# Kernel tuning notes

Hardware: AMD Instinct MI355X
Metric: run time of the kernel (lower is better)

The kernel has to match this reference:

```python
import jax, jax.numpy as jnp
import numpy as np
from jax import lax

B, N, C = 16, 131072, 3
NPOINT = 1024
OUT = 384
HID = OUT // 2


def farthest_point_sample(points, npoint):
    """points: [B, N, 3] -> idx: [B, npoint] int32 (classic FPS, start at index 0)."""
    b, n, _ = points.shape

    def body(carry, _):
        min_dist, last_idx = carry
        last = jnp.take_along_axis(points, last_idx[:, None, None], axis=1)  # [B,1,3]
        d = jnp.sum((points - last) ** 2, axis=-1)                           # [B,N]
        min_dist = jnp.minimum(min_dist, d)
        nxt = jnp.argmax(min_dist, axis=-1).astype(jnp.int32)
        return (min_dist, nxt), nxt

    idx0 = jnp.zeros((b,), jnp.int32)
    dist0 = jnp.full((b, n), 1e10, dtype=points.dtype)
    _, idxs = lax.scan(body, (dist0, idx0), None, length=npoint - 1)  # [npoint-1, B]
    return jnp.concatenate([idx0[None, :], idxs], axis=0).T           # [B, npoint]


def shared_mlp(x, w1, b1, w2, b2):
    # Conv1d(kernel_size=1) == pointwise linear; x: [B, M, Cin]
    h = jax.nn.gelu(jnp.einsum('bmc,ch->bmh', x, w1) + b1, approximate=False)
    return jnp.einsum('bmh,ho->bmo', h, w2) + b2


def setup_inputs() -> dict:
    key = jax.random.key(0)
    ks = jax.random.split(key, 9)
    points = jax.random.normal(ks[0], (B, N, C), dtype=jnp.float32)
    s1 = 1.0 / np.sqrt(C)
    s2 = 1.0 / np.sqrt(HID)
    return {
        'points': points,
        'w1t': jax.random.uniform(ks[1], (C, HID), jnp.float32, -s1, s1),
        'b1t': jax.random.uniform(ks[2], (HID,), jnp.float32, -s1, s1),
        'w2t': jax.random.uniform(ks[3], (HID, OUT), jnp.float32, -s2, s2),
        'b2t': jax.random.uniform(ks[4], (OUT,), jnp.float32, -s2, s2),
        'w1p': jax.random.uniform(ks[5], (C, HID), jnp.float32, -s1, s1),
        'b1p': jax.random.uniform(ks[6], (HID,), jnp.float32, -s1, s1),
        'w2p': jax.random.uniform(ks[7], (HID, OUT), jnp.float32, -s2, s2),
        'b2p': jax.random.uniform(ks[8], (OUT,), jnp.float32, -s2, s2),
    }


def reference(points, w1t, b1t, w2t, b2t, w1p, b1p, w2p, b2p):
    center_idx = farthest_point_sample(points, NPOINT)                      # [B, npoint]
    center = jnp.take_along_axis(points, center_idx[:, :, None], axis=1)   # [B, npoint, 3]
    det_token = shared_mlp(center, w1t, b1t, w2t, b2t)                      # [B, npoint, OUT]
    det_pos = shared_mlp(center, w1p, b1p, w2p, b2p)                        # [B, npoint, OUT]
    return det_token, det_pos
```

## Files before the change

### kernel.cpp

```cpp
#include <hip/hip_runtime.h>

#define NB 16
#define NPTS 131072
#define NPOINT 1024
#define HID 192
#define OUTC 384
#define BLKS_PER_B 16
#define THREADS_FPS 1024
#define PTS_PER_T 8
#define TAG_INIT 1023u
#define TAGM 0x3FFu

static __device__ __forceinline__ unsigned long long ald_ag(const unsigned long long* p) {
  return __hip_atomic_load(p, __ATOMIC_RELAXED, __HIP_MEMORY_SCOPE_AGENT);
}
static __device__ __forceinline__ void ast_ag(unsigned long long* p, unsigned long long v) {
  __hip_atomic_store(p, v, __ATOMIC_RELAXED, __HIP_MEMORY_SCOPE_AGENT);
}
__device__ __forceinline__ unsigned long long shfl_u64(unsigned long long v, int src) {
  unsigned int lo = (unsigned int)v, hi = (unsigned int)(v >> 32);
  lo = __shfl(lo, src, 64);
  hi = __shfl(hi, src, 64);
  return ((unsigned long long)hi << 32) | lo;
}
__device__ __forceinline__ unsigned long long shflxor_max_u64(unsigned long long v, int off) {
  unsigned int lo = (unsigned int)v, hi = (unsigned int)(v >> 32);
  lo = __shfl_xor(lo, off, 64);
  hi = __shfl_xor(hi, off, 64);
  unsigned long long o = ((unsigned long long)hi << 32) | lo;
  return o > v ? o : v;
}

__global__ __launch_bounds__(1024) void fps_kernel(
    const float* __restrict__ points,
    unsigned long long* __restrict__ slots,
    int* __restrict__ fps_idx)
{
  const int blk = blockIdx.x;
  const int b = blk >> 4;
  const int r = blk & 15;
  const int t = threadIdx.x;
  const int lane = t & 63, wid = t >> 6;
  const float* __restrict__ P = points + (size_t)b * NPTS * 3;
  const int base = r << 13;

  float px[PTS_PER_T], py[PTS_PER_T], pz[PTS_PER_T], md[PTS_PER_T];
#pragma unroll
  for (int k = 0; k < PTS_PER_T; ++k) {
    int i = base + (k << 10) + t;
    const float* pp = P + (size_t)i * 3;
    px[k] = pp[0]; py[k] = pp[1]; pz[k] = pp[2];
    md[k] = 1e10f;
  }

  float lx = P[0], ly = P[1], lz = P[2];

  __shared__ unsigned long long s_red[16];
  __shared__ float s_x[16], s_y[16], s_z[16];
  __shared__ float s_w[3];

  unsigned long long* region_b = slots + (size_t)b * 2 * 64;

  for (int it = 0; it < NPOINT - 1; ++it) {
    const int par = it & 1;
    const unsigned int uit = (unsigned int)it;
    const unsigned long long tg = (unsigned long long)uit;

    float bm = -1.0f; int bk = 0;
#pragma unroll
    for (int k = 0; k < PTS_PER_T; ++k) {
      float dx = px[k] - lx, dy = py[k] - ly, dz = pz[k] - lz;
      float d = __fadd_rn(__fadd_rn(__fmul_rn(dx, dx), __fmul_rn(dy, dy)), __fmul_rn(dz, dz));
      float m = fminf(md[k], d);
      md[k] = m;
      if (m > bm) { bm = m; bk = k; }
    }
    int bi = base + (bk << 10) + t;
    unsigned long long key = ((unsigned long long)__float_as_uint(bm) << 32)
                           | ((unsigned long long)(unsigned)(NPTS - 1 - bi) << 15);
#pragma unroll
    for (int off = 32; off > 0; off >>= 1) {
      unsigned int lo = (unsigned int)key, hi = (unsigned int)(key >> 32);
      lo = __shfl_down(lo, off, 64);
      hi = __shfl_down(hi, off, 64);
      unsigned long long o = ((unsigned long long)hi << 32) | lo;
      key = o > key ? o : key;
    }
    key = shfl_u64(key, 0);
    {
      int iw = NPTS - 1 - (int)((key >> 15) & 0x1FFFFull);
      int tw = (iw - base) & 1023;
      int kw = (iw - base) >> 10;
      float xc = px[0], yc = py[0], zc = pz[0];
#pragma unroll
      for (int k = 1; k < PTS_PER_T; ++k) {
        bool s = (kw == k);
        xc = s ? px[k] : xc; yc = s ? py[k] : yc; zc = s ? pz[k] : zc;
      }
      float xw = __shfl(xc, tw & 63, 64);
      float yw = __shfl(yc, tw & 63, 64);
      float zw = __shfl(zc, tw & 63, 64);
      if (lane == 0) {
        s_red[wid] = key;
        s_x[wid] = xw; s_y[wid] = yw; s_z[wid] = zw;
      }
    }
    __syncthreads();

    if (wid == 0) {
      unsigned long long kk = 0ull;
      if (lane < 16) {
        kk = s_red[lane];
#pragma unroll
        for (int off = 8; off > 0; off >>= 1) kk = shflxor_max_u64(kk, off);
      }
      kk = shfl_u64(kk, 0);
      int ib = NPTS - 1 - (int)((kk >> 15) & 0x1FFFFull);
      int wb = ((ib - base) & 1023) >> 6;
      unsigned long long* reg = region_b + (size_t)par * 64;
      if (lane < 4) {
        float cw = (lane == 1) ? s_x[wb] : (lane == 2) ? s_y[wb] : s_z[wb];
        unsigned long long w = (lane == 0)
            ? (kk | tg)
            : (((unsigned long long)__float_as_uint(cw) << 32) | tg);
        ast_ag(&reg[4 * r + lane], w);
      }
      unsigned long long* pp = reg + lane;
      unsigned long long pv;
      for (;;) {
        unsigned long long a0 = ald_ag(pp);
        unsigned long long a1 = ald_ag(pp);
        if (__ballot(((unsigned int)a0 & TAGM) == uit) == ~0ull) { pv = a0; break; }
        if (__ballot(((unsigned int)a1 & TAGM) == uit) == ~0ull) { pv = a1; break; }
        __builtin_amdgcn_s_sleep(2);
      }
      unsigned long long k4 = shfl_u64(pv, lane & ~3);
      k4 = shflxor_max_u64(k4, 4);
      k4 = shflxor_max_u64(k4, 8);
      k4 = shflxor_max_u64(k4, 16);
      k4 = shflxor_max_u64(k4, 32);
      int gi = NPTS - 1 - (int)((k4 >> 15) & 0x1FFFFull);
      int gr = gi >> 13;
      float myf = __uint_as_float((unsigned int)(pv >> 32));
      float nx = __shfl(myf, 4 * gr + 1, 64);
      float ny = __shfl(myf, 4 * gr + 2, 64);
      float nz = __shfl(myf, 4 * gr + 3, 64);
      if (lane == 0) {
        s_w[0] = nx; s_w[1] = ny; s_w[2] = nz;
        if (r == 0) fps_idx[b * NPOINT + it + 1] = gi;
      }
    }
    __syncthreads();
    lx = s_w[0]; ly = s_w[1]; lz = s_w[2];
  }
}

__global__ void fps_init_kernel(unsigned long long* __restrict__ slots,
                                int* __restrict__ fps_idx)
{
  int i = blockIdx.x * blockDim.x + threadIdx.x;
  if (i < NB * 2 * 64) slots[i] = (unsigned long long)TAG_INIT;
  if (i < NB) fps_idx[i * NPOINT] = 0;
}

__global__ __launch_bounds__(384) void mlp_kernel(
    const float* __restrict__ points,
    const int* __restrict__ fps_idx,
    const float* __restrict__ w1t, const float* __restrict__ b1t,
    const float* __restrict__ w2t, const float* __restrict__ b2t,
    const float* __restrict__ w1p, const float* __restrict__ b1p,
    const float* __restrict__ w2p, const float* __restrict__ b2p,
    float* __restrict__ out)
{
  __shared__ float s_c[4][3];
  __shared__ float s_h[2][HID][4];
  const int t = threadIdx.x;
  const int m0 = blockIdx.x * 4;
  if (t < 4) {
    int m = m0 + t;
    int b = m >> 10;
    int idx = fps_idx[m];
    const float* p = points + ((size_t)b * NPTS + (size_t)idx) * 3;
    s_c[t][0] = p[0]; s_c[t][1] = p[1]; s_c[t][2] = p[2];
  }
  __syncthreads();
  {
    const int mlp = t / HID;
    const int k = t - mlp * HID;
    const float* w1 = mlp ? w1p : w1t;
    const float* b1 = mlp ? b1p : b1t;
    float wa = w1[k], wb = w1[HID + k], wc = w1[2 * HID + k], bb = b1[k];
#pragma unroll
    for (int r = 0; r < 4; ++r) {
      float z = s_c[r][0] * wa + s_c[r][1] * wb + s_c[r][2] * wc + bb;
      float g = 0.5f * z * (1.0f + erff(z * 0.70710678118654752440f));
      s_h[mlp][k][r] = g;
    }
  }
  __syncthreads();
  const int o = t;
  float acct[4] = {0.f, 0.f, 0.f, 0.f};
  float accp[4] = {0.f, 0.f, 0.f, 0.f};
  const float* w2t_o = w2t + o;
  const float* w2p_o = w2p + o;
#pragma unroll 4
  for (int k = 0; k < HID; ++k) {
    float wt = w2t_o[(size_t)k * OUTC];
    float wp = w2p_o[(size_t)k * OUTC];
    float4 ht = *(const float4*)&s_h[0][k][0];
    float4 hp = *(const float4*)&s_h[1][k][0];
    acct[0] = fmaf(ht.x, wt, acct[0]);
    acct[1] = fmaf(ht.y, wt, acct[1]);
    acct[2] = fmaf(ht.z, wt, acct[2]);
    acct[3] = fmaf(ht.w, wt, acct[3]);
    accp[0] = fmaf(hp.x, wp, accp[0]);
    accp[1] = fmaf(hp.y, wp, accp[1]);
    accp[2] = fmaf(hp.z, wp, accp[2]);
    accp[3] = fmaf(hp.w, wp, accp[3]);
  }
  float bt = b2t[o], bp = b2p[o];
  const size_t posoff = (size_t)NB * NPOINT * OUTC;
#pragma unroll
  for (int rr = 0; rr < 4; ++rr) {
    size_t m = (size_t)(m0 + rr);
    out[m * OUTC + o] = acct[rr] + bt;
    out[posoff + m * OUTC + o] = accp[rr] + bp;
  }
}

extern "C" void kernel_launch(void* const* d_in, const int* in_sizes, int n_in,
                              void* d_out, int out_size, void* d_ws, size_t ws_size,
                              hipStream_t stream)
{
  const float* points = (const float*)d_in[0];
  const float* w1t = (const float*)d_in[1];
  const float* b1t = (const float*)d_in[2];
  const float* w2t = (const float*)d_in[3];
  const float* b2t = (const float*)d_in[4];
  const float* w1p = (const float*)d_in[5];
  const float* b1p = (const float*)d_in[6];
  const float* w2p = (const float*)d_in[7];
  const float* b2p = (const float*)d_in[8];
  float* out = (float*)d_out;

  char* ws = (char*)d_ws;
  unsigned long long* slots = (unsigned long long*)(ws + 0);
  int* fps_idx = (int*)(ws + 16384);

  hipLaunchKernelGGL(fps_init_kernel, dim3(8), dim3(256), 0, stream,
                     slots, fps_idx);

  void* args[3];
  args[0] = (void*)&points;
  args[1] = (void*)&slots;
  args[2] = (void*)&fps_idx;
  hipLaunchCooperativeKernel((void*)fps_kernel, dim3(NB * BLKS_PER_B),
                             dim3(THREADS_FPS), args, 0, stream);

  hipLaunchKernelGGL(mlp_kernel, dim3(NB * NPOINT / 4), dim3(384), 0, stream,
                     points, fps_idx, w1t, b1t, w2t, b2t, w1p, b1p, w2p, b2p, out);
}
```

Before: 3.160 ms.

## Exchange only argmax keys across blocks and reload winner coordinates from memory

Blocks no longer publish the winning point's coordinates alongside the key. Each block writes one 64-bit key slot, polls 16 slots with 16 lanes and no sleep, then reloads the winner's xyz from global memory by index. This shrinks the cross-block exchange and removes the per-wave coordinate selection and shuffles. In exchange it adds a dependent global load on the critical path of every iteration, and the tight spin without sleep may add memory traffic.

```diff
diff --git a/kernel.cpp b/kernel.cpp
--- a/kernel.cpp
+++ b/kernel.cpp
@@ -56,10 +56,9 @@
   float lx = P[0], ly = P[1], lz = P[2];
 
   __shared__ unsigned long long s_red[16];
-  __shared__ float s_x[16], s_y[16], s_z[16];
-  __shared__ float s_w[3];
-
-  unsigned long long* region_b = slots + (size_t)b * 2 * 64;
+  __shared__ int s_i;
+
+  unsigned long long* region_b = slots + (size_t)b * 2 * 16;
 
   for (int it = 0; it < NPOINT - 1; ++it) {
     const int par = it & 1;
@@ -86,72 +85,43 @@
       unsigned long long o = ((unsigned long long)hi << 32) | lo;
       key = o > key ? o : key;
     }
-    key = shfl_u64(key, 0);
-    {
-      int iw = NPTS - 1 - (int)((key >> 15) & 0x1FFFFull);
-      int tw = (iw - base) & 1023;
-      int kw = (iw - base) >> 10;
-      float xc = px[0], yc = py[0], zc = pz[0];
-#pragma unroll
-      for (int k = 1; k < PTS_PER_T; ++k) {
-        bool s = (kw == k);
-        xc = s ? px[k] : xc; yc = s ? py[k] : yc; zc = s ? pz[k] : zc;
-      }
-      float xw = __shfl(xc, tw & 63, 64);
-      float yw = __shfl(yc, tw & 63, 64);
-      float zw = __shfl(zc, tw & 63, 64);
-      if (lane == 0) {
-        s_red[wid] = key;
-        s_x[wid] = xw; s_y[wid] = yw; s_z[wid] = zw;
-      }
-    }
+    if (lane == 0) s_red[wid] = key;
     __syncthreads();
 
     if (wid == 0) {
+      unsigned long long* reg = region_b + (size_t)par * 16;
       unsigned long long kk = 0ull;
       if (lane < 16) {
         kk = s_red[lane];
-#pragma unroll
-        for (int off = 8; off > 0; off >>= 1) kk = shflxor_max_u64(kk, off);
+        kk = shflxor_max_u64(kk, 8);
+        kk = shflxor_max_u64(kk, 4);
+        kk = shflxor_max_u64(kk, 2);
+        kk = shflxor_max_u64(kk, 1);
+        if (lane == 0) ast_ag(&reg[r], kk | tg);
+        unsigned long long* pw = reg + lane;
+        unsigned long long pv;
+        for (;;) {
+          unsigned long long a0 = ald_ag(pw);
+          unsigned long long a1 = ald_ag(pw);
+          if (((unsigned int)a0 & TAGM) == uit) { pv = a0; break; }
+          if (((unsigned int)a1 & TAGM) == uit) { pv = a1; break; }
+        }
+        pv = shflxor_max_u64(pv, 8);
+        pv = shflxor_max_u64(pv, 4);
+        pv = shflxor_max_u64(pv, 2);
+        pv = shflxor_max_u64(pv, 1);
+        int gi = NPTS - 1 - (int)((pv >> 15) & 0x1FFFFull);
+        if (lane == 0) {
+          s_i = gi;
+          if (r == 0) fps_idx[b * NPOINT + it + 1] = gi;
+        }
       }
-      kk = shfl_u64(kk, 0);
-      int ib = NPTS - 1 - (int)((kk >> 15) & 0x1FFFFull);
-      int wb = ((ib - base) & 1023) >> 6;
-      unsigned long long* reg = region_b + (size_t)par * 64;
-      if (lane < 4) {
-        float cw = (lane == 1) ? s_x[wb] : (lane == 2) ? s_y[wb] : s_z[wb];
-        unsigned long long w = (lane == 0)
-            ? (kk | tg)
-            : (((unsigned long long)__float_as_uint(cw) << 32) | tg);
-        ast_ag(&reg[4 * r + lane], w);
-      }
-      unsigned long long* pp = reg + lane;
-      unsigned long long pv;
-      for (;;) {
-        unsigned long long a0 = ald_ag(pp);
-        unsigned long long a1 = ald_ag(pp);
-        if (__ballot(((unsigned int)a0 & TAGM) == uit) == ~0ull) { pv = a0; break; }
-        if (__ballot(((unsigned int)a1 & TAGM) == uit) == ~0ull) { pv = a1; break; }
-        __builtin_amdgcn_s_sleep(2);
-      }
-      unsigned long long k4 = shfl_u64(pv, lane & ~3);
-      k4 = shflxor_max_u64(k4, 4);
-      k4 = shflxor_max_u64(k4, 8);
-      k4 = shflxor_max_u64(k4, 16);
-      k4 = shflxor_max_u64(k4, 32);
-      int gi = NPTS - 1 - (int)((k4 >> 15) & 0x1FFFFull);
-      int gr = gi >> 13;
-      float myf = __uint_as_float((unsigned int)(pv >> 32));
-      float nx = __shfl(myf, 4 * gr + 1, 64);
-      float ny = __shfl(myf, 4 * gr + 2, 64);
-      float nz = __shfl(myf, 4 * gr + 3, 64);
-      if (lane == 0) {
-        s_w[0] = nx; s_w[1] = ny; s_w[2] = nz;
-        if (r == 0) fps_idx[b * NPOINT + it + 1] = gi;
-      }
     }
     __syncthreads();
-    lx = s_w[0]; ly = s_w[1]; lz = s_w[2];
+    {
+      const float* lp = P + (size_t)s_i * 3;
+      lx = lp[0]; ly = lp[1]; lz = lp[2];
+    }
   }
 }
 
@@ -159,7 +129,7 @@
                                 int* __restrict__ fps_idx)
 {
   int i = blockIdx.x * blockDim.x + threadIdx.x;
-  if (i < NB * 2 * 64) slots[i] = (unsigned long long)TAG_INIT;
+  if (i < NB * 2 * 16) slots[i] = (unsigned long long)TAG_INIT;
   if (i < NB) fps_idx[i * NPOINT] = 0;
 }
 
@@ -245,9 +215,9 @@
 
   char* ws = (char*)d_ws;
   unsigned long long* slots = (unsigned long long*)(ws + 0);
-  int* fps_idx = (int*)(ws + 16384);
-
-  hipLaunchKernelGGL(fps_init_kernel, dim3(8), dim3(256), 0, stream,
+  int* fps_idx = (int*)(ws + 4096);
+
+  hipLaunchKernelGGL(fps_init_kernel, dim3(2), dim3(256), 0, stream,
                      slots, fps_idx);
 
   void* args[3];
```

New measurement: 2.575 ms. 18.5% less time.
